# Kernel tuning notes

Hardware: AMD Instinct MI355X
Metric: run time of the kernel (lower is better)

## Reference

```python
import jax, jax.numpy as jnp
import numpy as np

B, LQ, LK, H = 4, 512, 512, 256


def setup_inputs() -> dict:
    key = jax.random.key(0)
    ks = jax.random.split(key, 8)
    s = 1.0 / np.sqrt(H)  # torch Linear init scale
    return {
        "query": jax.random.normal(ks[0], (B, LQ, H), dtype=jnp.float32),
        "values": jax.random.normal(ks[1], (B, LK, H), dtype=jnp.float32),
        "Wq": jax.random.uniform(ks[2], (H, H), jnp.float32, -s, s),
        "bq": jax.random.uniform(ks[3], (H,), jnp.float32, -s, s),
        "Wk": jax.random.uniform(ks[4], (H, H), jnp.float32, -s, s),
        "bk": jax.random.uniform(ks[5], (H,), jnp.float32, -s, s),
        "We": jax.random.uniform(ks[6], (H,), jnp.float32, -s, s),
        "be": jax.random.uniform(ks[7], (1,), jnp.float32, -s, s),
    }


def reference(query, values, Wq, bq, Wk, bk, We, be):
    # Linear projections (torch: x @ W.T + b)
    q = jnp.einsum("bqh,oh->bqo", query, Wq) + bq      # (B, Lq, H)
    k = jnp.einsum("bkh,oh->bko", values, Wk) + bk     # (B, Lk, H)
    # Additive attention energy: (B, Lq, Lk, H) broadcast add + tanh
    energy = jnp.tanh(q[:, :, None, :] + k[:, None, :, :])
    # energy_layer: Linear(H -> 1), squeeze -> scores (B, Lq, Lk)
    scores = jnp.einsum("bqkh,h->bqk", energy, We) + be[0]
    attention = jax.nn.softmax(scores, axis=-1)         # (B, Lq, Lk)
    context = jnp.einsum("bqk,bkh->bqh", attention, values)  # (B, Lq, H)
    return context, attention
```

## Files before the change

kernel.cpp:

```cpp
#include <hip/hip_runtime.h>


#define SCALE2 2.8853900817779268f

#if defined(__has_builtin)
#if __has_builtin(__builtin_amdgcn_exp2f)
#define FEXP2(x) __builtin_amdgcn_exp2f(x)
#endif
#if __has_builtin(__builtin_amdgcn_rcpf)
#define FRCP(x) __builtin_amdgcn_rcpf(x)
#endif
#endif
#ifndef FEXP2
#define FEXP2(x) exp2f(x)
#endif
#ifndef FRCP
#define FRCP(x) (1.0f/(x))
#endif

__global__ __launch_bounds__(512) void proj_kernel(
    const float* __restrict__ Q, const float* __restrict__ V,
    const float* __restrict__ Wq, const float* __restrict__ bq,
    const float* __restrict__ Wk, const float* __restrict__ bk,
    float* __restrict__ EqT, float* __restrict__ EkT)
{
  const int n0 = blockIdx.x * 64;
  const int o0 = blockIdx.y * 64;
  const bool isK = (blockIdx.z == 1);
  const float* X    = isK ? V  : Q;
  const float* W    = isK ? Wk : Wq;
  const float* bias = isK ? bk : bq;
  const int t  = threadIdx.x;
  const int tx = t & 15;
  const int ty = t >> 4;
  __shared__ float Xst[32][68];
  __shared__ float Wst[32][68];
  float acc[2][4] = {};
  const int sr = t >> 3, sc = (t & 7) << 2;
  float4 xv = *(const float4*)(X + (size_t)(n0 + sr) * 256 + sc);
  float4 wv = *(const float4*)(W + (size_t)(o0 + sr) * 256 + sc);
  for (int h0 = 0; h0 < 256; h0 += 32) {
    __syncthreads();
    Xst[sc  ][sr] = xv.x; Xst[sc+1][sr] = xv.y; Xst[sc+2][sr] = xv.z; Xst[sc+3][sr] = xv.w;
    Wst[sc  ][sr] = wv.x; Wst[sc+1][sr] = wv.y; Wst[sc+2][sr] = wv.z; Wst[sc+3][sr] = wv.w;
    __syncthreads();
    if (h0 < 224) {
      xv = *(const float4*)(X + (size_t)(n0 + sr) * 256 + h0 + 32 + sc);
      wv = *(const float4*)(W + (size_t)(o0 + sr) * 256 + h0 + 32 + sc);
    }
#pragma unroll 8
    for (int hh = 0; hh < 32; ++hh) {
      float2 a  = *(const float2*)&Xst[hh][ty*2];
      float4 bb = *(const float4*)&Wst[hh][tx*4];
      acc[0][0] = fmaf(a.x, bb.x, acc[0][0]); acc[0][1] = fmaf(a.x, bb.y, acc[0][1]);
      acc[0][2] = fmaf(a.x, bb.z, acc[0][2]); acc[0][3] = fmaf(a.x, bb.w, acc[0][3]);
      acc[1][0] = fmaf(a.y, bb.x, acc[1][0]); acc[1][1] = fmaf(a.y, bb.y, acc[1][1]);
      acc[1][2] = fmaf(a.y, bb.z, acc[1][2]); acc[1][3] = fmaf(a.y, bb.w, acc[1][3]);
    }
  }
  const float4 bv = *(const float4*)(bias + o0 + tx*4);
  float e[2][4];
#pragma unroll
  for (int i = 0; i < 2; ++i) {
    e[i][0] = FEXP2(SCALE2 * (acc[i][0] + bv.x));
    e[i][1] = FEXP2(SCALE2 * (acc[i][1] + bv.y));
    e[i][2] = FEXP2(SCALE2 * (acc[i][2] + bv.z));
    e[i][3] = FEXP2(SCALE2 * (acc[i][3] + bv.w));
  }
  float* outT = isK ? EkT : EqT;
  const int b  = n0 >> 9;
  const int nl = (n0 & 511) + ty*2;
#pragma unroll
  for (int j = 0; j < 4; ++j) {
    float2 st = {e[0][j], e[1][j]};
    *(float2*)(outT + (size_t)b*131072 + (size_t)(o0 + tx*4 + j)*512 + nl) = st;
  }
}

__global__ __launch_bounds__(256) void scores_kernel(
    const float* __restrict__ EqT, const float* __restrict__ EkT,
    const float* __restrict__ We, float* __restrict__ pt)
{
  const int flat = blockIdx.x;
  const int u = flat & 7, v = flat >> 3;
  const int z  = u*2 + (v >> 6);
  const int qt = (v >> 3) & 7;
  const int kt = v & 7;
  const int b = z >> 2, half = z & 3;
  const int h0 = half * 64;
  const int t  = threadIdx.x;
  const int qr = t >> 4;
  const int kr = t & 15;

  __shared__ float qsT[64][64];
  __shared__ float ks [64][64];

  const float* eqb = EqT + (size_t)b*131072 + (size_t)h0*512 + qt*64;
  const float* ekb = EkT + (size_t)b*131072 + (size_t)h0*512 + kt*64;

#pragma unroll
  for (int rep = 0; rep < 4; ++rep) {
    int idx = rep*256 + t;
    int r = idx >> 4, c = (idx & 15) << 2;
    *(float4*)&qsT[r][c] = *(const float4*)(eqb + (size_t)r*512 + c);
    *(float4*)&ks [r][c] = *(const float4*)(ekb + (size_t)r*512 + c);
  }
  __syncthreads();

  float a[4][4];
#pragma unroll
  for (int i = 0; i < 4; ++i)
#pragma unroll
    for (int j = 0; j < 4; ++j) a[i][j] = 0.f;

#pragma unroll 4
  for (int hh = 0; hh < 64; ++hh) {
    const float w = We[h0 + hh];
    const float4 qv = *(const float4*)&qsT[hh][qr*4];
    const float4 kv = *(const float4*)&ks [hh][kr*4];
    const float qa[4] = {qv.x, qv.y, qv.z, qv.w};
#pragma unroll
    for (int i = 0; i < 4; ++i) {
      float x0 = fmaf(qa[i], kv.x, 1.0f);
      float x1 = fmaf(qa[i], kv.y, 1.0f);
      float x2 = fmaf(qa[i], kv.z, 1.0f);
      float x3 = fmaf(qa[i], kv.w, 1.0f);
      float p01 = x0 * x1, p23 = x2 * x3;
      float r4  = FRCP(p01 * p23);
      float wr  = w * r4;
      float sw  = wr * p23, uw = wr * p01;
      a[i][0] = fmaf(sw, x1, a[i][0]);
      a[i][1] = fmaf(sw, x0, a[i][1]);
      a[i][2] = fmaf(uw, x3, a[i][2]);
      a[i][3] = fmaf(uw, x2, a[i][3]);
    }
  }

  float* sout = pt + (size_t)half*1048576
                   + (size_t)(b*512 + qt*64 + qr*4)*512 + kt*64 + kr*4;
#pragma unroll
  for (int i = 0; i < 4; ++i) {
    float4 st = {a[i][0], a[i][1], a[i][2], a[i][3]};
    *(float4*)(sout + (size_t)i*512) = st;
  }
}

__global__ __launch_bounds__(512) void ctx_kernel(
    const float* __restrict__ values, const float* __restrict__ pt,
    float* __restrict__ attn, float* __restrict__ ctx)
{
  const int t    = threadIdx.x;
  const int row0 = blockIdx.x * 8;
  const int b    = row0 >> 9;
  __shared__ float ts[8][512];
  __shared__ float red[8][8][256];

#pragma unroll
  for (int rep = 0; rep < 2; ++rep) {
    int idx = rep*512 + t;
    int r = idx >> 7, c = (idx & 127) << 2;
    size_t off = (size_t)(row0 + r)*512 + c;
    float4 v0 = *(const float4*)(pt + off);
    float4 v1 = *(const float4*)(pt + 1048576 + off);
    float4 v2 = *(const float4*)(pt + 2097152 + off);
    float4 v3 = *(const float4*)(pt + 3145728 + off);
    float4 s = {v0.x+v1.x+v2.x+v3.x, v0.y+v1.y+v2.y+v3.y,
                v0.z+v1.z+v2.z+v3.z, v0.w+v1.w+v2.w+v3.w};
    *(float4*)&ts[r][c] = s;
  }
  __syncthreads();

  const int w = t >> 6, j = t & 63;
  {
    float v[8];
    float mn = 1e30f;
#pragma unroll
    for (int i = 0; i < 8; ++i) { v[i] = ts[w][j + 64*i]; mn = fminf(mn, v[i]); }
#pragma unroll
    for (int off = 32; off > 0; off >>= 1) mn = fminf(mn, __shfl_xor(mn, off, 64));
    float sum = 0.f;
#pragma unroll
    for (int i = 0; i < 8; ++i) { v[i] = FEXP2((mn - v[i]) * SCALE2); sum += v[i]; }
#pragma unroll
    for (int off = 32; off > 0; off >>= 1) sum += __shfl_xor(sum, off, 64);
    const float inv = 1.0f / sum;
    float* gp = attn + (size_t)(row0 + w) * 512 + j;
#pragma unroll
    for (int i = 0; i < 8; ++i) {
      float p = v[i] * inv;
      ts[w][j + 64*i] = p;
      gp[64*i] = p;
    }
  }
  __syncthreads();

  const int h4 = j << 2;
  const int wk0 = w * 64;
  const float* vwb = values + (size_t)b*131072 + (size_t)wk0*256 + h4;
  float4 acc[8];
#pragma unroll
  for (int r = 0; r < 8; ++r) acc[r] = (float4){0,0,0,0};

  float4 cv[4], nv[4];
#pragma unroll
  for (int jj = 0; jj < 4; ++jj) cv[jj] = *(const float4*)(vwb + (size_t)jj*256);

  for (int kq = 0; kq < 16; ++kq) {
    if (kq < 15) {
#pragma unroll
      for (int jj = 0; jj < 4; ++jj)
        nv[jj] = *(const float4*)(vwb + (size_t)((kq+1)*4 + jj)*256);
    }
    float4 a[8];
#pragma unroll
    for (int r = 0; r < 8; ++r) a[r] = *(const float4*)&ts[r][wk0 + kq*4];
#pragma unroll
    for (int jj = 0; jj < 4; ++jj) {
      float4 v4 = cv[jj];
#pragma unroll
      for (int r = 0; r < 8; ++r) {
        float ar = (jj == 0) ? a[r].x : (jj == 1) ? a[r].y : (jj == 2) ? a[r].z : a[r].w;
        acc[r].x = fmaf(ar, v4.x, acc[r].x);
        acc[r].y = fmaf(ar, v4.y, acc[r].y);
        acc[r].z = fmaf(ar, v4.z, acc[r].z);
        acc[r].w = fmaf(ar, v4.w, acc[r].w);
      }
    }
#pragma unroll
    for (int jj = 0; jj < 4; ++jj) cv[jj] = nv[jj];
  }

#pragma unroll
  for (int r = 0; r < 8; ++r) *(float4*)&red[w][r][h4] = acc[r];
  __syncthreads();
  {
    const int rr = t >> 6;
    const int hh4 = (t & 63) << 2;
    float4 s = *(const float4*)&red[0][rr][hh4];
#pragma unroll
    for (int ww = 1; ww < 8; ++ww) {
      float4 p = *(const float4*)&red[ww][rr][hh4];
      s.x += p.x; s.y += p.y; s.z += p.z; s.w += p.w;
    }
    *(float4*)(ctx + (size_t)(row0 + rr)*256 + hh4) = s;
  }
}

extern "C" void kernel_launch(void* const* d_in, const int* in_sizes, int n_in,
                              void* d_out, int out_size, void* d_ws, size_t ws_size,
                              hipStream_t stream)
{
  const float* query  = (const float*)d_in[0];
  const float* values = (const float*)d_in[1];
  const float* Wq     = (const float*)d_in[2];
  const float* bq     = (const float*)d_in[3];
  const float* Wk     = (const float*)d_in[4];
  const float* bk     = (const float*)d_in[5];
  const float* We     = (const float*)d_in[6];

  float* ctx  = (float*)d_out;
  float* attn = ctx + 4*512*256;
  float* EqT  = (float*)d_ws;
  float* EkT  = EqT + 524288;
  float* pt   = EkT + 524288;

  proj_kernel  <<<dim3(32, 4, 2), 512, 0, stream>>>(query, values, Wq, bq, Wk, bk, EqT, EkT);
  scores_kernel<<<1024, 256, 0, stream>>>(EqT, EkT, We, pt);
  ctx_kernel   <<<256, 512, 0, stream>>>(values, pt, attn, ctx);
}
```

Baseline: 65.00 us.

## Enlarge scores tile to 128x128 with two-stage h-chunk shared-memory prefetch

The scores kernel now handles a 128x128 q-by-k tile per block with 512 threads and 4x8 outputs per thread, so there are 256 blocks instead of 1024. The 64-wide h slice is split into two 32-row chunks, and the second chunk's global loads are issued into registers before computing on the first. This aims to improve data reuse per shared-memory load and to hide global latency. In exchange there are fewer blocks for 256 CUs, a single wave of work, and higher register pressure from the 32 accumulators plus prefetch registers.

```diff
diff --git a/kernel.cpp b/kernel.cpp
--- a/kernel.cpp
+++ b/kernel.cpp
@@ -77,71 +77,106 @@
   }
 }
 
-__global__ __launch_bounds__(256) void scores_kernel(
+__global__ __launch_bounds__(512) void scores_kernel(
     const float* __restrict__ EqT, const float* __restrict__ EkT,
     const float* __restrict__ We, float* __restrict__ pt)
 {
   const int flat = blockIdx.x;
-  const int u = flat & 7, v = flat >> 3;
-  const int z  = u*2 + (v >> 6);
-  const int qt = (v >> 3) & 7;
-  const int kt = v & 7;
+  const int kt = flat & 3;
+  const int qt = (flat >> 2) & 3;
+  const int z  = flat >> 4;
   const int b = z >> 2, half = z & 3;
   const int h0 = half * 64;
   const int t  = threadIdx.x;
   const int qr = t >> 4;
   const int kr = t & 15;
 
-  __shared__ float qsT[64][64];
-  __shared__ float ks [64][64];
-
-  const float* eqb = EqT + (size_t)b*131072 + (size_t)h0*512 + qt*64;
-  const float* ekb = EkT + (size_t)b*131072 + (size_t)h0*512 + kt*64;
-
-#pragma unroll
-  for (int rep = 0; rep < 4; ++rep) {
-    int idx = rep*256 + t;
-    int r = idx >> 4, c = (idx & 15) << 2;
-    *(float4*)&qsT[r][c] = *(const float4*)(eqb + (size_t)r*512 + c);
-    *(float4*)&ks [r][c] = *(const float4*)(ekb + (size_t)r*512 + c);
-  }
-  __syncthreads();
-
-  float a[4][4];
+  __shared__ float4 qs[2][32][32];
+  __shared__ float4 ks[2][32][32];
+
+  const float* eqb = EqT + (size_t)b*131072 + (size_t)h0*512 + qt*128;
+  const float* ekb = EkT + (size_t)b*131072 + (size_t)h0*512 + kt*128;
+
+  const int r0 = t >> 5, c0 = t & 31;
+  const int r1 = 16 + r0;
+
+  float4 aq0 = *(const float4*)(eqb + (size_t)r0*512 + c0*4);
+  float4 ak0 = *(const float4*)(ekb + (size_t)r0*512 + c0*4);
+  float4 aq1 = *(const float4*)(eqb + (size_t)r1*512 + c0*4);
+  float4 ak1 = *(const float4*)(ekb + (size_t)r1*512 + c0*4);
+  qs[0][r0][c0] = aq0; ks[0][r0][c0] = ak0;
+  qs[0][r1][c0] = aq1; ks[0][r1][c0] = ak1;
+
+  float4 bq0 = *(const float4*)(eqb + (size_t)(32 + r0)*512 + c0*4);
+  float4 bk0 = *(const float4*)(ekb + (size_t)(32 + r0)*512 + c0*4);
+  float4 bq1 = *(const float4*)(eqb + (size_t)(32 + r1)*512 + c0*4);
+  float4 bk1 = *(const float4*)(ekb + (size_t)(32 + r1)*512 + c0*4);
+
+  __syncthreads();
+
+  float a[4][8];
 #pragma unroll
   for (int i = 0; i < 4; ++i)
 #pragma unroll
-    for (int j = 0; j < 4; ++j) a[i][j] = 0.f;
-
-#pragma unroll 4
-  for (int hh = 0; hh < 64; ++hh) {
-    const float w = We[h0 + hh];
-    const float4 qv = *(const float4*)&qsT[hh][qr*4];
-    const float4 kv = *(const float4*)&ks [hh][kr*4];
-    const float qa[4] = {qv.x, qv.y, qv.z, qv.w};
-#pragma unroll
-    for (int i = 0; i < 4; ++i) {
-      float x0 = fmaf(qa[i], kv.x, 1.0f);
-      float x1 = fmaf(qa[i], kv.y, 1.0f);
-      float x2 = fmaf(qa[i], kv.z, 1.0f);
-      float x3 = fmaf(qa[i], kv.w, 1.0f);
-      float p01 = x0 * x1, p23 = x2 * x3;
-      float r4  = FRCP(p01 * p23);
-      float wr  = w * r4;
-      float sw  = wr * p23, uw = wr * p01;
-      a[i][0] = fmaf(sw, x1, a[i][0]);
-      a[i][1] = fmaf(sw, x0, a[i][1]);
-      a[i][2] = fmaf(uw, x3, a[i][2]);
-      a[i][3] = fmaf(uw, x2, a[i][3]);
-    }
-  }
+    for (int j = 0; j < 8; ++j) a[i][j] = 0.f;
+
+#define SCORES_COMPUTE(BUF, HBASE)                                          \
+  _Pragma("unroll 4")                                                       \
+  for (int hh = 0; hh < 32; ++hh) {                                         \
+    const float w = We[h0 + (HBASE) + hh];                                  \
+    const float4 qv  = qs[BUF][hh][qr];                                     \
+    const float4 kv0 = ks[BUF][hh][kr];                                     \
+    const float4 kv1 = ks[BUF][hh][kr + 16];                                \
+    const float qa[4] = {qv.x, qv.y, qv.z, qv.w};                           \
+    _Pragma("unroll")                                                       \
+    for (int i = 0; i < 4; ++i) {                                           \
+      {                                                                     \
+        float x0 = fmaf(qa[i], kv0.x, 1.0f);                                \
+        float x1 = fmaf(qa[i], kv0.y, 1.0f);                                \
+        float x2 = fmaf(qa[i], kv0.z, 1.0f);                                \
+        float x3 = fmaf(qa[i], kv0.w, 1.0f);                                \
+        float p01 = x0 * x1, p23 = x2 * x3;                                 \
+        float r4  = FRCP(p01 * p23);                                        \
+        float wr  = w * r4;                                                 \
+        float sw  = wr * p23, uw = wr * p01;                                \
+        a[i][0] = fmaf(sw, x1, a[i][0]);                                    \
+        a[i][1] = fmaf(sw, x0, a[i][1]);                                    \
+        a[i][2] = fmaf(uw, x3, a[i][2]);                                    \
+        a[i][3] = fmaf(uw, x2, a[i][3]);                                    \
+      }                                                                     \
+      {                                                                     \
+        float x0 = fmaf(qa[i], kv1.x, 1.0f);                                \
+        float x1 = fmaf(qa[i], kv1.y, 1.0f);                                \
+        float x2 = fmaf(qa[i], kv1.z, 1.0f);                                \
+        float x3 = fmaf(qa[i], kv1.w, 1.0f);                                \
+        float p01 = x0 * x1, p23 = x2 * x3;                                 \
+        float r4  = FRCP(p01 * p23);                                        \
+        float wr  = w * r4;                                                 \
+        float sw  = wr * p23, uw = wr * p01;                                \
+        a[i][4] = fmaf(sw, x1, a[i][4]);                                    \
+        a[i][5] = fmaf(sw, x0, a[i][5]);                                    \
+        a[i][6] = fmaf(uw, x3, a[i][6]);                                    \
+        a[i][7] = fmaf(uw, x2, a[i][7]);                                    \
+      }                                                                     \
+    }                                                                       \
+  }
+
+  SCORES_COMPUTE(0, 0)
+
+  qs[1][r0][c0] = bq0; ks[1][r0][c0] = bk0;
+  qs[1][r1][c0] = bq1; ks[1][r1][c0] = bk1;
+  __syncthreads();
+
+  SCORES_COMPUTE(1, 32)
 
   float* sout = pt + (size_t)half*1048576
-                   + (size_t)(b*512 + qt*64 + qr*4)*512 + kt*64 + kr*4;
+                   + (size_t)(b*512 + qt*128 + qr*4)*512 + kt*128 + kr*4;
 #pragma unroll
   for (int i = 0; i < 4; ++i) {
-    float4 st = {a[i][0], a[i][1], a[i][2], a[i][3]};
-    *(float4*)(sout + (size_t)i*512) = st;
+    float4 s0 = {a[i][0], a[i][1], a[i][2], a[i][3]};
+    float4 s1 = {a[i][4], a[i][5], a[i][6], a[i][7]};
+    *(float4*)(sout + (size_t)i*512) = s0;
+    *(float4*)(sout + (size_t)i*512 + 64) = s1;
   }
 }
 
@@ -265,6 +300,6 @@
   float* pt   = EkT + 524288;
 
   proj_kernel  <<<dim3(32, 4, 2), 512, 0, stream>>>(query, values, Wq, bq, Wk, bk, EqT, EkT);
-  scores_kernel<<<1024, 256, 0, stream>>>(EqT, EkT, We, pt);
+  scores_kernel<<<256, 512, 0, stream>>>(EqT, EkT, We, pt);
   ctx_kernel   <<<256, 512, 0, stream>>>(values, pt, attn, ctx);
 }
```

Result: slower. 68.26 us (+5.0%).

## Use packed FP32 math and 64x128 tiles with split-phase loads in scores kernel

Applied to the files above, without the earlier changes.

The scores kernel now computes two query rows at once with packed f32x2 FMAs and multiplies, which can map to packed FP32 VALU instructions. Each block now covers a 64x128 tile, so the grid drops to 512 blocks and every loaded query value is reused against twice as many keys. The 64-deep reduction is split into two 32-row halves, and the global loads for the second half are issued before the first half is computed so they overlap with it. In exchange the kernel uses more registers and runs fewer blocks, and the reciprocals are still scalar.

```diff
diff --git a/kernel.cpp b/kernel.cpp
--- a/kernel.cpp
+++ b/kernel.cpp
@@ -17,6 +17,30 @@
 #ifndef FRCP
 #define FRCP(x) (1.0f/(x))
 #endif
+
+typedef float f32x2 __attribute__((ext_vector_type(2)));
+
+static __device__ __forceinline__ f32x2 pk2(float lo, float hi) {
+  f32x2 r; r.x = lo; r.y = hi; return r;
+}
+
+static __device__ __forceinline__ void pk_quad_step(
+    const f32x2 qp, const float4 kv, const float w, f32x2 acc[4])
+{
+  const f32x2 one2 = pk2(1.0f, 1.0f);
+  f32x2 x0 = __builtin_elementwise_fma(qp, pk2(kv.x, kv.x), one2);
+  f32x2 x1 = __builtin_elementwise_fma(qp, pk2(kv.y, kv.y), one2);
+  f32x2 x2 = __builtin_elementwise_fma(qp, pk2(kv.z, kv.z), one2);
+  f32x2 x3 = __builtin_elementwise_fma(qp, pk2(kv.w, kv.w), one2);
+  f32x2 p01 = x0 * x1, p23 = x2 * x3, P = p01 * p23;
+  f32x2 rr; rr.x = FRCP(P.x); rr.y = FRCP(P.y);
+  f32x2 wr = rr * w;
+  f32x2 sw = wr * p23, uw = wr * p01;
+  acc[0] = __builtin_elementwise_fma(sw, x1, acc[0]);
+  acc[1] = __builtin_elementwise_fma(sw, x0, acc[1]);
+  acc[2] = __builtin_elementwise_fma(uw, x3, acc[2]);
+  acc[3] = __builtin_elementwise_fma(uw, x2, acc[3]);
+}
 
 __global__ __launch_bounds__(512) void proj_kernel(
     const float* __restrict__ Q, const float* __restrict__ V,
@@ -82,66 +106,101 @@
     const float* __restrict__ We, float* __restrict__ pt)
 {
   const int flat = blockIdx.x;
-  const int u = flat & 7, v = flat >> 3;
-  const int z  = u*2 + (v >> 6);
-  const int qt = (v >> 3) & 7;
-  const int kt = v & 7;
+  const int kt = flat & 3;
+  const int qt = (flat >> 2) & 7;
+  const int z  = flat >> 5;
   const int b = z >> 2, half = z & 3;
   const int h0 = half * 64;
   const int t  = threadIdx.x;
   const int qr = t >> 4;
   const int kr = t & 15;
 
-  __shared__ float qsT[64][64];
-  __shared__ float ks [64][64];
+  __shared__ float4 qs4[2][32][16];
+  __shared__ float4 ks4[2][32][32];
 
   const float* eqb = EqT + (size_t)b*131072 + (size_t)h0*512 + qt*64;
-  const float* ekb = EkT + (size_t)b*131072 + (size_t)h0*512 + kt*64;
-
-#pragma unroll
-  for (int rep = 0; rep < 4; ++rep) {
-    int idx = rep*256 + t;
-    int r = idx >> 4, c = (idx & 15) << 2;
-    *(float4*)&qsT[r][c] = *(const float4*)(eqb + (size_t)r*512 + c);
-    *(float4*)&ks [r][c] = *(const float4*)(ekb + (size_t)r*512 + c);
-  }
-  __syncthreads();
-
-  float a[4][4];
-#pragma unroll
-  for (int i = 0; i < 4; ++i)
-#pragma unroll
-    for (int j = 0; j < 4; ++j) a[i][j] = 0.f;
+  const float* ekb = EkT + (size_t)b*131072 + (size_t)h0*512 + kt*128;
+
+  const int rs = t >> 3;
+  const int sq = (t & 7) * 2;
+  const int sk = (t & 7) * 4;
+
+  float4 aq0 = *(const float4*)(eqb + (size_t)rs*512 + (sq  )*4);
+  float4 aq1 = *(const float4*)(eqb + (size_t)rs*512 + (sq+1)*4);
+  float4 ak[4];
+#pragma unroll
+  for (int j = 0; j < 4; ++j)
+    ak[j] = *(const float4*)(ekb + (size_t)rs*512 + (sk+j)*4);
+  qs4[0][rs][sq] = aq0; qs4[0][rs][sq+1] = aq1;
+#pragma unroll
+  for (int j = 0; j < 4; ++j) ks4[0][rs][sk+j] = ak[j];
+
+  float4 bq0 = *(const float4*)(eqb + (size_t)(32+rs)*512 + (sq  )*4);
+  float4 bq1 = *(const float4*)(eqb + (size_t)(32+rs)*512 + (sq+1)*4);
+  float4 bk[4];
+#pragma unroll
+  for (int j = 0; j < 4; ++j)
+    bk[j] = *(const float4*)(ekb + (size_t)(32+rs)*512 + (sk+j)*4);
+
+  __syncthreads();
+
+  f32x2 acc[2][2][4];
+#pragma unroll
+  for (int p = 0; p < 2; ++p)
+#pragma unroll
+    for (int c = 0; c < 2; ++c)
+#pragma unroll
+      for (int j = 0; j < 4; ++j) acc[p][c][j] = pk2(0.f, 0.f);
 
 #pragma unroll 4
-  for (int hh = 0; hh < 64; ++hh) {
+  for (int hh = 0; hh < 32; ++hh) {
     const float w = We[h0 + hh];
-    const float4 qv = *(const float4*)&qsT[hh][qr*4];
-    const float4 kv = *(const float4*)&ks [hh][kr*4];
-    const float qa[4] = {qv.x, qv.y, qv.z, qv.w};
-#pragma unroll
-    for (int i = 0; i < 4; ++i) {
-      float x0 = fmaf(qa[i], kv.x, 1.0f);
-      float x1 = fmaf(qa[i], kv.y, 1.0f);
-      float x2 = fmaf(qa[i], kv.z, 1.0f);
-      float x3 = fmaf(qa[i], kv.w, 1.0f);
-      float p01 = x0 * x1, p23 = x2 * x3;
-      float r4  = FRCP(p01 * p23);
-      float wr  = w * r4;
-      float sw  = wr * p23, uw = wr * p01;
-      a[i][0] = fmaf(sw, x1, a[i][0]);
-      a[i][1] = fmaf(sw, x0, a[i][1]);
-      a[i][2] = fmaf(uw, x3, a[i][2]);
-      a[i][3] = fmaf(uw, x2, a[i][3]);
-    }
+    const float4 qv  = qs4[0][hh][qr];
+    const float4 kv0 = ks4[0][hh][kr];
+    const float4 kv1 = ks4[0][hh][kr + 16];
+    const f32x2 qlo = pk2(qv.x, qv.y), qhi = pk2(qv.z, qv.w);
+    pk_quad_step(qlo, kv0, w, acc[0][0]);
+    pk_quad_step(qlo, kv1, w, acc[0][1]);
+    pk_quad_step(qhi, kv0, w, acc[1][0]);
+    pk_quad_step(qhi, kv1, w, acc[1][1]);
+  }
+
+  qs4[1][rs][sq] = bq0; qs4[1][rs][sq+1] = bq1;
+#pragma unroll
+  for (int j = 0; j < 4; ++j) ks4[1][rs][sk+j] = bk[j];
+  __syncthreads();
+
+#pragma unroll 4
+  for (int hh = 0; hh < 32; ++hh) {
+    const float w = We[h0 + 32 + hh];
+    const float4 qv  = qs4[1][hh][qr];
+    const float4 kv0 = ks4[1][hh][kr];
+    const float4 kv1 = ks4[1][hh][kr + 16];
+    const f32x2 qlo = pk2(qv.x, qv.y), qhi = pk2(qv.z, qv.w);
+    pk_quad_step(qlo, kv0, w, acc[0][0]);
+    pk_quad_step(qlo, kv1, w, acc[0][1]);
+    pk_quad_step(qhi, kv0, w, acc[1][0]);
+    pk_quad_step(qhi, kv1, w, acc[1][1]);
   }
 
   float* sout = pt + (size_t)half*1048576
-                   + (size_t)(b*512 + qt*64 + qr*4)*512 + kt*64 + kr*4;
-#pragma unroll
-  for (int i = 0; i < 4; ++i) {
-    float4 st = {a[i][0], a[i][1], a[i][2], a[i][3]};
-    *(float4*)(sout + (size_t)i*512) = st;
+                   + (size_t)(b*512 + qt*64 + qr*4)*512 + kt*128 + kr*4;
+#pragma unroll
+  for (int p = 0; p < 2; ++p) {
+#pragma unroll
+    for (int s = 0; s < 2; ++s) {
+      const int i = p*2 + s;
+      float4 s0, s1;
+      if (s == 0) {
+        s0 = (float4){acc[p][0][0].x, acc[p][0][1].x, acc[p][0][2].x, acc[p][0][3].x};
+        s1 = (float4){acc[p][1][0].x, acc[p][1][1].x, acc[p][1][2].x, acc[p][1][3].x};
+      } else {
+        s0 = (float4){acc[p][0][0].y, acc[p][0][1].y, acc[p][0][2].y, acc[p][0][3].y};
+        s1 = (float4){acc[p][1][0].y, acc[p][1][1].y, acc[p][1][2].y, acc[p][1][3].y};
+      }
+      *(float4*)(sout + (size_t)i*512) = s0;
+      *(float4*)(sout + (size_t)i*512 + 64) = s1;
+    }
   }
 }
 
@@ -265,6 +324,6 @@
   float* pt   = EkT + 524288;
 
   proj_kernel  <<<dim3(32, 4, 2), 512, 0, stream>>>(query, values, Wq, bq, Wk, bk, EqT, EkT);
-  scores_kernel<<<1024, 256, 0, stream>>>(EqT, EkT, We, pt);
+  scores_kernel<<<512, 256, 0, stream>>>(EqT, EkT, We, pt);
   ctx_kernel   <<<256, 512, 0, stream>>>(values, pt, attn, ctx);
 }
```

Result: faster. 60.20 us (-7.4%).
